# Kernel optimization log

Measured on AMD Instinct MI355X. Metric: run time of the kernel, lower is better.

The kernel has to match this reference:

```python
import jax, jax.numpy as jnp
import numpy as np

PAIR = 128
HID = 64
EPS = 1e-5


def _ln(x, w, b):
    mu = jnp.mean(x, axis=-1, keepdims=True)
    var = jnp.mean((x - mu) ** 2, axis=-1, keepdims=True)
    return (x - mu) * jax.lax.rsqrt(var + EPS) * w + b


def setup_inputs() -> dict:
    key = jax.random.key(0)
    ks = jax.random.split(key, 8)
    B, N = 1, 448
    s_in = 1.0 / np.sqrt(PAIR)
    s_h = 1.0 / np.sqrt(HID)
    return {
        "z": jax.random.normal(ks[0], (B, N, N, PAIR), jnp.float32),
        "z_mask": jnp.ones((B, N, N), jnp.float32),
        "ln_w": jnp.ones((PAIR,), jnp.float32),
        "ln_b": jnp.zeros((PAIR,), jnp.float32),
        "lnh_w": jnp.ones((HID,), jnp.float32),
        "lnh_b": jnp.zeros((HID,), jnp.float32),
        "g1_w": jax.random.uniform(ks[1], (PAIR, HID), jnp.float32, -s_in, s_in),
        "g1_b": jnp.zeros((HID,), jnp.float32),
        "g2_w": jax.random.uniform(ks[2], (PAIR, HID), jnp.float32, -s_in, s_in),
        "g2_b": jnp.zeros((HID,), jnp.float32),
        "l1_w": jax.random.uniform(ks[3], (PAIR, HID), jnp.float32, -s_in, s_in),
        "l1_b": jnp.zeros((HID,), jnp.float32),
        "l2_w": jax.random.uniform(ks[4], (PAIR, HID), jnp.float32, -s_in, s_in),
        "l2_b": jnp.zeros((HID,), jnp.float32),
        "eg_w": jax.random.uniform(ks[5], (PAIR, PAIR), jnp.float32, -s_in, s_in),
        "eg_b": jnp.zeros((PAIR,), jnp.float32),
        "out_w": jax.random.uniform(ks[6], (HID, PAIR), jnp.float32, -s_h, s_h),
        "out_b": jnp.zeros((PAIR,), jnp.float32),
    }


def reference(z, z_mask, ln_w, ln_b, lnh_w, lnh_b, g1_w, g1_b, g2_w, g2_b,
              l1_w, l1_b, l2_w, l2_b, eg_w, eg_b, out_w, out_b):
    m = z_mask[..., None]                      # [B,N,N,1]
    zn = _ln(z, ln_w, ln_b)                    # [B,N,N,P]
    ab1 = jax.nn.sigmoid(zn @ g1_w + g1_b) * (zn @ l1_w + l1_b) * m  # [B,N,N,H]
    ab2 = jax.nn.sigmoid(zn @ g2_w + g2_b) * (zn @ l2_w + l2_b) * m  # [B,N,N,H]
    # outgoing + incoming triangle products, per channel c
    block = (jnp.einsum('bikc,bjkc->bijc', ab1, ab2)
             + jnp.einsum('bkic,bkjc->bijc', ab1, ab2))              # [B,N,N,H]
    out = jax.nn.sigmoid(zn @ eg_w + eg_b) * (_ln(block, lnh_w, lnh_b) @ out_w + out_b) * m
    return out
```

## Files before the change

kernel.cpp:

```cpp
#include <hip/hip_runtime.h>
#include <stdint.h>

#define N 448
#define NN (N*N)
#define P 128
#define H 64
#define PN 512
#define CH (PN*N)

typedef __attribute__((ext_vector_type(8))) short bf16x8;
typedef __attribute__((ext_vector_type(4))) float f32x4;

__device__ __forceinline__ ushort f2bf(float f) {
    uint u = __builtin_bit_cast(uint, f);
    uint r = u + 0x7FFFu + ((u >> 16) & 1u);
    return (ushort)(r >> 16);
}
__device__ __forceinline__ float bf2f(ushort h) {
    uint u = ((uint)h) << 16;
    return __builtin_bit_cast(float, u);
}
__device__ __forceinline__ float sigmoidf(float x) {
    return 1.0f / (1.0f + __expf(-x));
}

__global__ void k_prep(const float* __restrict__ g1w, const float* __restrict__ l1w,
                       const float* __restrict__ g2w, const float* __restrict__ l2w,
                       const float* __restrict__ egw,
                       ushort* __restrict__ wfrag) {
    int idx = blockIdx.x*256 + threadIdx.x;
    for (int e = idx; e < 24*4*64*8; e += gridDim.x*256) {
        int b  = e & 7;
        int l  = (e >> 3) & 63;
        int ks = (e >> 9) & 3;
        int ct = e >> 11;
        int k   = ks*32 + 8*(l>>4) + b;
        int col = ct*16 + (l & 15);
        float v;
        if (col < 64)       v = g1w[k*64 + col];
        else if (col < 128) v = l1w[k*64 + col - 64];
        else if (col < 192) v = g2w[k*64 + col - 128];
        else if (col < 256) v = l2w[k*64 + col - 192];
        else                v = egw[k*128 + col - 256];
        wfrag[e] = f2bf(v);
    }
}

__global__ __launch_bounds__(256) void k_proj(
    const float* __restrict__ z, const float* __restrict__ mask,
    const float* __restrict__ lnw, const float* __restrict__ lnb,
    const float* __restrict__ g1b, const float* __restrict__ l1b,
    const float* __restrict__ g2b, const float* __restrict__ l2b,
    const float* __restrict__ egb,
    const ushort* __restrict__ wfrag,
    ushort* __restrict__ abt, ushort* __restrict__ gsig)
{
    __shared__ ushort zn[64*128];
    __shared__ ushort gs[64][136];
    const int t = threadIdx.x;
    const int w = t >> 6, l = t & 63;
    const int i = blockIdx.x / 7, j0 = (blockIdx.x % 7) * 64;

    {
        const int p = t >> 2;
        const int q = t & 3;
        const float* zp = z + (size_t)(i*N + j0 + p)*P + q*32;
        float4 v[8];
        #pragma unroll
        for (int x = 0; x < 8; ++x) v[x] = *(const float4*)(zp + x*4);
        float s = 0.f, sq = 0.f;
        #pragma unroll
        for (int x = 0; x < 8; ++x) {
            s  += v[x].x + v[x].y + v[x].z + v[x].w;
            sq += v[x].x*v[x].x + v[x].y*v[x].y + v[x].z*v[x].z + v[x].w*v[x].w;
        }
        s += __shfl_xor(s, 1);  sq += __shfl_xor(sq, 1);
        s += __shfl_xor(s, 2);  sq += __shfl_xor(sq, 2);
        float mu   = s * (1.0f/128.0f);
        float var  = sq * (1.0f/128.0f) - mu*mu;
        float rstd = rsqrtf(var + 1e-5f);
        #pragma unroll
        for (int cc = 0; cc < 4; ++cc) {
            int chunk = q*4 + cc;
            const float* lwp = lnw + chunk*8;
            const float* lbp = lnb + chunk*8;
            float4 lwa = *(const float4*)(lwp), lwb = *(const float4*)(lwp+4);
            float4 lba = *(const float4*)(lbp), lbb = *(const float4*)(lbp+4);
            float4 va = v[cc*2], vb = v[cc*2+1];
            float n0 = (va.x - mu)*rstd*lwa.x + lba.x;
            float n1 = (va.y - mu)*rstd*lwa.y + lba.y;
            float n2 = (va.z - mu)*rstd*lwa.z + lba.z;
            float n3 = (va.w - mu)*rstd*lwa.w + lba.w;
            float n4 = (vb.x - mu)*rstd*lwb.x + lbb.x;
            float n5 = (vb.y - mu)*rstd*lwb.y + lbb.y;
            float n6 = (vb.z - mu)*rstd*lwb.z + lbb.z;
            float n7 = (vb.w - mu)*rstd*lwb.w + lbb.w;
            uint4 pk;
            pk.x = (uint)f2bf(n0) | ((uint)f2bf(n1) << 16);
            pk.y = (uint)f2bf(n2) | ((uint)f2bf(n3) << 16);
            pk.z = (uint)f2bf(n4) | ((uint)f2bf(n5) << 16);
            pk.w = (uint)f2bf(n6) | ((uint)f2bf(n7) << 16);
            uint boff = (uint)p*256u + (((uint)(chunk ^ (p & 7)) & 15u) << 4);
            *(uint4*)((char*)zn + boff) = pk;
        }
    }
    __syncthreads();

    const int half = w & 1, pair = w >> 1;
    const uint lr = l & 15, lk = l >> 4;
    const float* mrow = mask + (size_t)i*N + j0;
    const float* gb = pair ? g2b : g1b;
    const float* lb = pair ? l2b : l1b;

    #pragma unroll 1
    for (int sub = 0; sub < 2; ++sub) {
        const int ctg = pair*8 + half*2 + sub;
        const int ctl = ctg + 4;
        f32x4 ag[4], al[4];
        #pragma unroll
        for (int mi = 0; mi < 4; ++mi) { ag[mi] = (f32x4){0,0,0,0}; al[mi] = (f32x4){0,0,0,0}; }

        #pragma unroll
        for (int ks = 0; ks < 4; ++ks) {
            bf16x8 bg = *(const bf16x8*)(wfrag + ((size_t)(ctg*4 + ks)*64 + l)*8);
            bf16x8 blf = *(const bf16x8*)(wfrag + ((size_t)(ctl*4 + ks)*64 + l)*8);
            #pragma unroll
            for (int mi = 0; mi < 4; ++mi) {
                uint row = mi*16u + lr;
                uint chunk = (uint)(ks*4) + lk;
                bf16x8 af = *(const bf16x8*)((const char*)zn + row*256u + (((chunk ^ (row & 7u)) & 15u) << 4));
                ag[mi] = __builtin_amdgcn_mfma_f32_16x16x32_bf16(af, bg,  ag[mi], 0,0,0);
                al[mi] = __builtin_amdgcn_mfma_f32_16x16x32_bf16(af, blf, al[mi], 0,0,0);
            }
        }

        const int cidx = (half*2 + sub)*16 + (int)lr;
        const float gbias = gb[cidx];
        const float lbias = lb[cidx];
        #pragma unroll
        for (int mi = 0; mi < 4; ++mi) {
            float mv[4];
            #pragma unroll
            for (int r = 0; r < 4; ++r) mv[r] = mrow[mi*16 + (int)lk*4 + r];
            ushort4 pk;
            float o0 = sigmoidf(ag[mi][0] + gbias) * (al[mi][0] + lbias) * mv[0];
            float o1 = sigmoidf(ag[mi][1] + gbias) * (al[mi][1] + lbias) * mv[1];
            float o2 = sigmoidf(ag[mi][2] + gbias) * (al[mi][2] + lbias) * mv[2];
            float o3 = sigmoidf(ag[mi][3] + gbias) * (al[mi][3] + lbias) * mv[3];
            pk.x = f2bf(o0); pk.y = f2bf(o1); pk.z = f2bf(o2); pk.w = f2bf(o3);
            size_t off = (size_t)(pair*64 + cidx)*CH + (size_t)i*N + j0 + mi*16 + (int)lk*4;
            *(ushort4*)(abt + off) = pk;
        }
    }

    {
        f32x4 ae[4][2];
        #pragma unroll
        for (int mi = 0; mi < 4; ++mi) { ae[mi][0] = (f32x4){0,0,0,0}; ae[mi][1] = (f32x4){0,0,0,0}; }

        #pragma unroll
        for (int ks = 0; ks < 4; ++ks) {
            bf16x8 b0 = *(const bf16x8*)(wfrag + ((size_t)((16 + w*2)*4 + ks)*64 + l)*8);
            bf16x8 b1 = *(const bf16x8*)(wfrag + ((size_t)((17 + w*2)*4 + ks)*64 + l)*8);
            #pragma unroll
            for (int mi = 0; mi < 4; ++mi) {
                uint row = mi*16u + lr;
                uint chunk = (uint)(ks*4) + lk;
                bf16x8 af = *(const bf16x8*)((const char*)zn + row*256u + (((chunk ^ (row & 7u)) & 15u) << 4));
                ae[mi][0] = __builtin_amdgcn_mfma_f32_16x16x32_bf16(af, b0, ae[mi][0], 0,0,0);
                ae[mi][1] = __builtin_amdgcn_mfma_f32_16x16x32_bf16(af, b1, ae[mi][1], 0,0,0);
            }
        }

        float biasB[2];
        biasB[0] = egb[w*32 + (int)lr];
        biasB[1] = egb[w*32 + 16 + (int)lr];
        #pragma unroll
        for (int mi = 0; mi < 4; ++mi) {
            float mv[4];
            #pragma unroll
            for (int r = 0; r < 4; ++r) mv[r] = mrow[mi*16 + (int)lk*4 + r];
            #pragma unroll
            for (int e = 0; e < 2; ++e) {
                int cg = w*32 + e*16 + (int)lr;
                #pragma unroll
                for (int r = 0; r < 4; ++r) {
                    float sg = sigmoidf(ae[mi][e][r] + biasB[e]) * mv[r];
                    gs[mi*16 + (int)lk*4 + r][cg] = f2bf(sg);
                }
            }
        }
    }
    __syncthreads();

    {
        int p2 = t >> 2, q2 = t & 3;
        size_t pos = (size_t)(i*N + j0 + p2);
        #pragma unroll
        for (int s2 = 0; s2 < 4; ++s2) {
            uint4 vv = *(const uint4*)((const char*)&gs[p2][0] + q2*64 + s2*16);
            *(uint4*)(gsig + pos*128 + q2*32 + s2*8) = vv;
        }
    }
}

__global__ __launch_bounds__(256) void k_transpose(const ushort* __restrict__ abt,
                                                   ushort* __restrict__ abtt) {
    int bid = blockIdx.x;
    int tile = bid % 49, a = bid / 49;
    int y0 = (tile / 7) * 64, x0 = (tile % 7) * 64;
    const ushort* src = abt  + (size_t)a*CH;
    ushort*       dst = abtt + (size_t)a*CH;
    __shared__ ushort tl[64][68];
    int t = threadIdx.x;
    #pragma unroll
    for (int q = 0; q < 4; ++q) {
        int f = q*1024 + t*4;
        int r = f >> 6, c4 = f & 63;
        ushort4 v = *(const ushort4*)(src + (size_t)(y0 + r)*N + x0 + c4);
        tl[r][c4] = v.x; tl[r][c4+1] = v.y; tl[r][c4+2] = v.z; tl[r][c4+3] = v.w;
    }
    __syncthreads();
    #pragma unroll
    for (int q = 0; q < 4; ++q) {
        int f = q*1024 + t*4;
        int r = f >> 6, c4 = f & 63;
        ushort4 v;
        v.x = tl[c4][r]; v.y = tl[c4+1][r]; v.z = tl[c4+2][r]; v.w = tl[c4+3][r];
        *(ushort4*)(dst + (size_t)(x0 + r)*N + y0 + c4) = v;
    }
}

__global__ __launch_bounds__(512) void k_tri(const ushort* __restrict__ abt,
                                             const ushort* __restrict__ abtt,
                                             float* __restrict__ blk) {
    int bid = (blockIdx.x & 7)*128 + (blockIdx.x >> 3);
    const int c = bid >> 4;
    const int tij = bid & 15;
    const int i0 = (tij >> 2) * 128, j0 = (tij & 3) * 128;
    const int t = threadIdx.x, w = t >> 6, l = t & 63;
    const int wr = w >> 2, wc = w & 3;
    const uint lr = l & 15, lk = l >> 4;

    __shared__ ushort lds[4][128*64];

    const int tt = w >> 1;
    const ushort* basep = (tt >= 2) ? abtt : abt;
    const int chan = (tt & 1) ? 64 + c : c;
    const int r0   = (tt & 1) ? j0 : i0;
    const ushort* sbase = basep + (size_t)chan*CH + (size_t)r0*N;
    const int rhalf = (w & 1) * 64;

    f32x4 acc[4][2];
    #pragma unroll
    for (int a = 0; a < 4; ++a) { acc[a][0] = (f32x4){0,0,0,0}; acc[a][1] = (f32x4){0,0,0,0}; }

    for (int kk = 0; kk < 7; ++kk) {
        __syncthreads();
        const ushort* sb = sbase + kk*64;
        #pragma unroll
        for (int q = 0; q < 8; ++q) {
            int r  = rhalf + q*8 + (l >> 3);
            int ch = (l & 7) ^ (r & 7);
            const ushort* g = sb + (size_t)r*N + ch*8;
            __builtin_amdgcn_global_load_lds(
                (const __attribute__((address_space(1))) uint*)g,
                (__attribute__((address_space(3))) uint*)(&lds[tt][rhalf*64 + q*512]),
                16, 0, 0);
        }
        __syncthreads();

        #pragma unroll
        for (int ks = 0; ks < 2; ++ks) {
            const uint chunk = (uint)(ks*4) + lk;
            bf16x8 a1[4], b1[2];
            #pragma unroll
            for (int x = 0; x < 4; ++x) {
                uint rowa = (uint)wr*64u + (uint)x*16u + lr;
                a1[x] = *(const bf16x8*)((const char*)lds[0] + rowa*128u + (((chunk ^ (rowa & 7u)) & 15u) << 4));
            }
            #pragma unroll
            for (int x = 0; x < 2; ++x) {
                uint rowb = (uint)wc*32u + (uint)x*16u + lr;
                b1[x] = *(const bf16x8*)((const char*)lds[1] + rowb*128u + (((chunk ^ (rowb & 7u)) & 15u) << 4));
            }
            #pragma unroll
            for (int mi = 0; mi < 4; ++mi)
                #pragma unroll
                for (int nj = 0; nj < 2; ++nj)
                    acc[mi][nj] = __builtin_amdgcn_mfma_f32_16x16x32_bf16(a1[mi], b1[nj], acc[mi][nj], 0,0,0);

            bf16x8 a2[4], b2[2];
            #pragma unroll
            for (int x = 0; x < 4; ++x) {
                uint rowa = (uint)wr*64u + (uint)x*16u + lr;
                a2[x] = *(const bf16x8*)((const char*)lds[2] + rowa*128u + (((chunk ^ (rowa & 7u)) & 15u) << 4));
            }
            #pragma unroll
            for (int x = 0; x < 2; ++x) {
                uint rowb = (uint)wc*32u + (uint)x*16u + lr;
                b2[x] = *(const bf16x8*)((const char*)lds[3] + rowb*128u + (((chunk ^ (rowb & 7u)) & 15u) << 4));
            }
            #pragma unroll
            for (int mi = 0; mi < 4; ++mi)
                #pragma unroll
                for (int nj = 0; nj < 2; ++nj)
                    acc[mi][nj] = __builtin_amdgcn_mfma_f32_16x16x32_bf16(a2[mi], b2[nj], acc[mi][nj], 0,0,0);
        }
    }

    #pragma unroll
    for (int mi = 0; mi < 4; ++mi) {
        int ib = i0 + wr*64 + mi*16 + (int)lk*4;
        #pragma unroll
        for (int nj = 0; nj < 2; ++nj) {
            int jb = j0 + wc*32 + nj*16 + (int)lr;
            if (jb < N) {
                #pragma unroll
                for (int r = 0; r < 4; ++r) {
                    int ii = ib + r;
                    if (ii < N) blk[(size_t)c*NN + (size_t)ii*N + jb] = acc[mi][nj][r];
                }
            }
        }
    }
}

__global__ __launch_bounds__(256) void k_out(const float* __restrict__ blk,
    const ushort* __restrict__ gsig,
    const float* __restrict__ lnhw, const float* __restrict__ lnhb,
    const float* __restrict__ outw, const float* __restrict__ outb,
    float* __restrict__ out)
{
    __shared__ float sblk[64][68];
    const int t = threadIdx.x;
    const int w = t >> 6, l = t & 63;
    const int pos0 = blockIdx.x * 64;

    #pragma unroll
    for (int q = 0; q < 4; ++q) {
        int flat = q*256 + t;
        int h = flat >> 4, f4 = flat & 15;
        float4 v = *(const float4*)(blk + (size_t)h*NN + pos0 + f4*4);
        sblk[f4*4+0][h] = v.x;
        sblk[f4*4+1][h] = v.y;
        sblk[f4*4+2][h] = v.z;
        sblk[f4*4+3][h] = v.w;
    }
    __syncthreads();

    {
        int p = w*16 + (l >> 2);
        int sub = l & 3;
        float vv[16];
        float s = 0.f, sq = 0.f;
        #pragma unroll
        for (int j = 0; j < 16; ++j) {
            float x = sblk[p][sub*16 + j];
            vv[j] = x; s += x; sq += x*x;
        }
        s += __shfl_xor(s, 1);  sq += __shfl_xor(sq, 1);
        s += __shfl_xor(s, 2);  sq += __shfl_xor(sq, 2);
        float mu   = s * (1.0f/64.0f);
        float var  = sq * (1.0f/64.0f) - mu*mu;
        float rstd = rsqrtf(var + 1e-5f);
        #pragma unroll
        for (int j = 0; j < 16; ++j) {
            float nv = (vv[j] - mu)*rstd*lnhw[sub*16+j] + lnhb[sub*16+j];
            sblk[p][sub*16 + j] = nv;
        }
    }
    __syncthreads();

    const int c4 = (t & 31) * 4;
    const int pg = t >> 5;
    float4 ob = *(const float4*)(outb + c4);

    #pragma unroll 1
    for (int hh = 0; hh < 2; ++hh) {
        const int prow = hh*32 + pg*4;
        float acc[4][4];
        #pragma unroll
        for (int j2 = 0; j2 < 4; ++j2)
            #pragma unroll
            for (int cc = 0; cc < 4; ++cc) acc[j2][cc] = 0.f;

        #pragma unroll 4
        for (int h4 = 0; h4 < 16; ++h4) {
            float4 wv[4];
            #pragma unroll
            for (int j = 0; j < 4; ++j)
                wv[j] = *(const float4*)(outw + (h4*4+j)*128 + c4);
            #pragma unroll
            for (int j2 = 0; j2 < 4; ++j2) {
                float4 av = *(const float4*)(&sblk[prow + j2][h4*4]);
                acc[j2][0] += av.x*wv[0].x + av.y*wv[1].x + av.z*wv[2].x + av.w*wv[3].x;
                acc[j2][1] += av.x*wv[0].y + av.y*wv[1].y + av.z*wv[2].y + av.w*wv[3].y;
                acc[j2][2] += av.x*wv[0].z + av.y*wv[1].z + av.z*wv[2].z + av.w*wv[3].z;
                acc[j2][3] += av.x*wv[0].w + av.y*wv[1].w + av.z*wv[2].w + av.w*wv[3].w;
            }
        }

        #pragma unroll
        for (int j2 = 0; j2 < 4; ++j2) {
            size_t pos = (size_t)(pos0 + prow + j2);
            ushort4 gv = *(const ushort4*)(gsig + pos*128 + c4);
            float4 res;
            res.x = bf2f(gv.x) * (acc[j2][0] + ob.x);
            res.y = bf2f(gv.y) * (acc[j2][1] + ob.y);
            res.z = bf2f(gv.z) * (acc[j2][2] + ob.z);
            res.w = bf2f(gv.w) * (acc[j2][3] + ob.w);
            *(float4*)(out + pos*128 + c4) = res;
        }
    }
}

extern "C" void kernel_launch(void* const* d_in, const int* in_sizes, int n_in,
                              void* d_out, int out_size, void* d_ws, size_t ws_size,
                              hipStream_t stream) {
    const float* z    = (const float*)d_in[0];
    const float* mask = (const float*)d_in[1];
    const float* lnw  = (const float*)d_in[2];
    const float* lnb  = (const float*)d_in[3];
    const float* lnhw = (const float*)d_in[4];
    const float* lnhb = (const float*)d_in[5];
    const float* g1w  = (const float*)d_in[6];
    const float* g1b  = (const float*)d_in[7];
    const float* g2w  = (const float*)d_in[8];
    const float* g2b  = (const float*)d_in[9];
    const float* l1w  = (const float*)d_in[10];
    const float* l1b  = (const float*)d_in[11];
    const float* l2w  = (const float*)d_in[12];
    const float* l2b  = (const float*)d_in[13];
    const float* egw  = (const float*)d_in[14];
    const float* egb  = (const float*)d_in[15];
    const float* outw = (const float*)d_in[16];
    const float* outb = (const float*)d_in[17];

    char* ws = (char*)d_ws;
    const size_t SZ_AB = (size_t)2*64*CH*2;
    const size_t SZ_G  = (size_t)NN*128*2;
    const size_t SZ_BL = (size_t)64*NN*4;
    ushort* abt    = (ushort*)ws;
    ushort* abtt   = (ushort*)(ws + SZ_AB);
    ushort* gsig   = (ushort*)(ws + 2*SZ_AB);
    float*  blkb   = (float*) (ws + 2*SZ_AB + SZ_G);
    ushort* wfrag  = (ushort*)(ws + 2*SZ_AB + SZ_G + SZ_BL);

    k_prep<<<32, 256, 0, stream>>>(g1w, l1w, g2w, l2w, egw, wfrag);
    k_proj<<<3136, 256, 0, stream>>>(z, mask, lnw, lnb, g1b, l1b, g2b, l2b, egb, wfrag, abt, gsig);
    k_transpose<<<128*49, 256, 0, stream>>>(abt, abtt);
    k_tri<<<64*16, 512, 0, stream>>>(abt, abtt, blkb);
    k_out<<<NN/64, 256, 0, stream>>>(blkb, gsig, lnhw, lnhb, outw, outb, (float*)d_out);
}
```

Baseline: 297.7 us.

## Enlarge per-wave tile in triangle kernel and streamline projection epilogues

The triangle-product kernel now runs 256 threads per block instead of 512. Each wave computes a 64x64 output tile (4x4 MFMA accumulators) rather than 64x32, which raises MFMA-to-LDS-read reuse and removes the cross-wave split of the staging loads. In the projection kernel, the manual bf16 rounding is replaced by the packed hardware convert instruction, mask loads become float4 vector loads, and the separate gating staging buffer is dropped by reusing the swizzled zn LDS region after an added barrier. The larger accumulator tile raises register pressure and halves threads per block, which may reduce occupancy or latency hiding.

Result: no change. 293.1 us (-1.6%).

```diff
diff --git a/kernel.cpp b/kernel.cpp
--- a/kernel.cpp
+++ b/kernel.cpp
@@ -22,6 +22,11 @@
 }
 __device__ __forceinline__ float sigmoidf(float x) {
     return 1.0f / (1.0f + __expf(-x));
+}
+__device__ __forceinline__ uint cvtpk(float lo, float hi) {
+    uint r;
+    asm("v_cvt_pk_bf16_f32 %0, %1, %2" : "=v"(r) : "v"(lo), "v"(hi));
+    return r;
 }
 
 __global__ void k_prep(const float* __restrict__ g1w, const float* __restrict__ l1w,
@@ -56,7 +61,6 @@
     ushort* __restrict__ abt, ushort* __restrict__ gsig)
 {
     __shared__ ushort zn[64*128];
-    __shared__ ushort gs[64][136];
     const int t = threadIdx.x;
     const int w = t >> 6, l = t & 63;
     const int i = blockIdx.x / 7, j0 = (blockIdx.x % 7) * 64;
@@ -96,10 +100,10 @@
             float n6 = (vb.z - mu)*rstd*lwb.z + lbb.z;
             float n7 = (vb.w - mu)*rstd*lwb.w + lbb.w;
             uint4 pk;
-            pk.x = (uint)f2bf(n0) | ((uint)f2bf(n1) << 16);
-            pk.y = (uint)f2bf(n2) | ((uint)f2bf(n3) << 16);
-            pk.z = (uint)f2bf(n4) | ((uint)f2bf(n5) << 16);
-            pk.w = (uint)f2bf(n6) | ((uint)f2bf(n7) << 16);
+            pk.x = cvtpk(n0, n1);
+            pk.y = cvtpk(n2, n3);
+            pk.z = cvtpk(n4, n5);
+            pk.w = cvtpk(n6, n7);
             uint boff = (uint)p*256u + (((uint)(chunk ^ (p & 7)) & 15u) << 4);
             *(uint4*)((char*)zn + boff) = pk;
         }
@@ -122,7 +126,7 @@
 
         #pragma unroll
         for (int ks = 0; ks < 4; ++ks) {
-            bf16x8 bg = *(const bf16x8*)(wfrag + ((size_t)(ctg*4 + ks)*64 + l)*8);
+            bf16x8 bg  = *(const bf16x8*)(wfrag + ((size_t)(ctg*4 + ks)*64 + l)*8);
             bf16x8 blf = *(const bf16x8*)(wfrag + ((size_t)(ctl*4 + ks)*64 + l)*8);
             #pragma unroll
             for (int mi = 0; mi < 4; ++mi) {
@@ -139,17 +143,16 @@
         const float lbias = lb[cidx];
         #pragma unroll
         for (int mi = 0; mi < 4; ++mi) {
-            float mv[4];
-            #pragma unroll
-            for (int r = 0; r < 4; ++r) mv[r] = mrow[mi*16 + (int)lk*4 + r];
-            ushort4 pk;
-            float o0 = sigmoidf(ag[mi][0] + gbias) * (al[mi][0] + lbias) * mv[0];
-            float o1 = sigmoidf(ag[mi][1] + gbias) * (al[mi][1] + lbias) * mv[1];
-            float o2 = sigmoidf(ag[mi][2] + gbias) * (al[mi][2] + lbias) * mv[2];
-            float o3 = sigmoidf(ag[mi][3] + gbias) * (al[mi][3] + lbias) * mv[3];
-            pk.x = f2bf(o0); pk.y = f2bf(o1); pk.z = f2bf(o2); pk.w = f2bf(o3);
+            float4 mv = *(const float4*)(mrow + mi*16 + (int)lk*4);
+            float o0 = sigmoidf(ag[mi][0] + gbias) * (al[mi][0] + lbias) * mv.x;
+            float o1 = sigmoidf(ag[mi][1] + gbias) * (al[mi][1] + lbias) * mv.y;
+            float o2 = sigmoidf(ag[mi][2] + gbias) * (al[mi][2] + lbias) * mv.z;
+            float o3 = sigmoidf(ag[mi][3] + gbias) * (al[mi][3] + lbias) * mv.w;
+            uint2 pk;
+            pk.x = cvtpk(o0, o1);
+            pk.y = cvtpk(o2, o3);
             size_t off = (size_t)(pair*64 + cidx)*CH + (size_t)i*N + j0 + mi*16 + (int)lk*4;
-            *(ushort4*)(abt + off) = pk;
+            *(uint2*)(abt + off) = pk;
         }
     }
 
@@ -172,21 +175,24 @@
             }
         }
 
+        __syncthreads();
+
         float biasB[2];
         biasB[0] = egb[w*32 + (int)lr];
         biasB[1] = egb[w*32 + 16 + (int)lr];
         #pragma unroll
         for (int mi = 0; mi < 4; ++mi) {
-            float mv[4];
-            #pragma unroll
-            for (int r = 0; r < 4; ++r) mv[r] = mrow[mi*16 + (int)lk*4 + r];
+            float4 mv = *(const float4*)(mrow + mi*16 + (int)lk*4);
+            float mva[4] = { mv.x, mv.y, mv.z, mv.w };
             #pragma unroll
             for (int e = 0; e < 2; ++e) {
-                int cg = w*32 + e*16 + (int)lr;
+                uint cg = (uint)(w*32 + e*16) + lr;
                 #pragma unroll
                 for (int r = 0; r < 4; ++r) {
-                    float sg = sigmoidf(ae[mi][e][r] + biasB[e]) * mv[r];
-                    gs[mi*16 + (int)lk*4 + r][cg] = f2bf(sg);
+                    float sg = sigmoidf(ae[mi][e][r] + biasB[e]) * mva[r];
+                    uint row = (uint)(mi*16) + lk*4u + (uint)r;
+                    uint boff = row*256u + (((((cg >> 3) ^ (row & 7u)) & 15u)) << 4) + ((cg & 7u) << 1);
+                    *(ushort*)((char*)zn + boff) = (ushort)cvtpk(sg, sg);
                 }
             }
         }
@@ -198,7 +204,9 @@
         size_t pos = (size_t)(i*N + j0 + p2);
         #pragma unroll
         for (int s2 = 0; s2 < 4; ++s2) {
-            uint4 vv = *(const uint4*)((const char*)&gs[p2][0] + q2*64 + s2*16);
+            int chunk = q2*4 + s2;
+            uint boff = (uint)p2*256u + (((uint)(chunk ^ (p2 & 7)) & 15u) << 4);
+            uint4 vv = *(const uint4*)((const char*)zn + boff);
             *(uint4*)(gsig + pos*128 + q2*32 + s2*8) = vv;
         }
     }
@@ -231,7 +239,7 @@
     }
 }
 
-__global__ __launch_bounds__(512) void k_tri(const ushort* __restrict__ abt,
+__global__ __launch_bounds__(256) void k_tri(const ushort* __restrict__ abt,
                                              const ushort* __restrict__ abtt,
                                              float* __restrict__ blk) {
     int bid = (blockIdx.x & 7)*128 + (blockIdx.x >> 3);
@@ -239,33 +247,33 @@
     const int tij = bid & 15;
     const int i0 = (tij >> 2) * 128, j0 = (tij & 3) * 128;
     const int t = threadIdx.x, w = t >> 6, l = t & 63;
-    const int wr = w >> 2, wc = w & 3;
+    const int wr = w >> 1, wc = w & 1;
     const uint lr = l & 15, lk = l >> 4;
 
     __shared__ ushort lds[4][128*64];
 
-    const int tt = w >> 1;
-    const ushort* basep = (tt >= 2) ? abtt : abt;
-    const int chan = (tt & 1) ? 64 + c : c;
-    const int r0   = (tt & 1) ? j0 : i0;
+    const ushort* basep = (w >= 2) ? abtt : abt;
+    const int chan = (w & 1) ? 64 + c : c;
+    const int r0   = (w & 1) ? j0 : i0;
     const ushort* sbase = basep + (size_t)chan*CH + (size_t)r0*N;
-    const int rhalf = (w & 1) * 64;
-
-    f32x4 acc[4][2];
+
+    f32x4 acc[4][4];
     #pragma unroll
-    for (int a = 0; a < 4; ++a) { acc[a][0] = (f32x4){0,0,0,0}; acc[a][1] = (f32x4){0,0,0,0}; }
+    for (int a = 0; a < 4; ++a)
+        #pragma unroll
+        for (int b = 0; b < 4; ++b) acc[a][b] = (f32x4){0.f,0.f,0.f,0.f};
 
     for (int kk = 0; kk < 7; ++kk) {
         __syncthreads();
         const ushort* sb = sbase + kk*64;
         #pragma unroll
-        for (int q = 0; q < 8; ++q) {
-            int r  = rhalf + q*8 + (l >> 3);
+        for (int q = 0; q < 16; ++q) {
+            int r  = q*8 + (l >> 3);
             int ch = (l & 7) ^ (r & 7);
             const ushort* g = sb + (size_t)r*N + ch*8;
             __builtin_amdgcn_global_load_lds(
                 (const __attribute__((address_space(1))) uint*)g,
-                (__attribute__((address_space(3))) uint*)(&lds[tt][rhalf*64 + q*512]),
+                (__attribute__((address_space(3))) uint*)(&lds[w][q*512]),
                 16, 0, 0);
         }
         __syncthreads();
@@ -273,38 +281,32 @@
         #pragma unroll
         for (int ks = 0; ks < 2; ++ks) {
             const uint chunk = (uint)(ks*4) + lk;
-            bf16x8 a1[4], b1[2];
+            bf16x8 a1[4], b1[4];
             #pragma unroll
             for (int x = 0; x < 4; ++x) {
                 uint rowa = (uint)wr*64u + (uint)x*16u + lr;
+                uint rowb = (uint)wc*64u + (uint)x*16u + lr;
                 a1[x] = *(const bf16x8*)((const char*)lds[0] + rowa*128u + (((chunk ^ (rowa & 7u)) & 15u) << 4));
-            }
-            #pragma unroll
-            for (int x = 0; x < 2; ++x) {
-                uint rowb = (uint)wc*32u + (uint)x*16u + lr;
                 b1[x] = *(const bf16x8*)((const char*)lds[1] + rowb*128u + (((chunk ^ (rowb & 7u)) & 15u) << 4));
             }
             #pragma unroll
             for (int mi = 0; mi < 4; ++mi)
                 #pragma unroll
-                for (int nj = 0; nj < 2; ++nj)
+                for (int nj = 0; nj < 4; ++nj)
                     acc[mi][nj] = __builtin_amdgcn_mfma_f32_16x16x32_bf16(a1[mi], b1[nj], acc[mi][nj], 0,0,0);
 
-            bf16x8 a2[4], b2[2];
+            bf16x8 a2[4], b2[4];
             #pragma unroll
             for (int x = 0; x < 4; ++x) {
                 uint rowa = (uint)wr*64u + (uint)x*16u + lr;
+                uint rowb = (uint)wc*64u + (uint)x*16u + lr;
                 a2[x] = *(const bf16x8*)((const char*)lds[2] + rowa*128u + (((chunk ^ (rowa & 7u)) & 15u) << 4));
-            }
-            #pragma unroll
-            for (int x = 0; x < 2; ++x) {
-                uint rowb = (uint)wc*32u + (uint)x*16u + lr;
                 b2[x] = *(const bf16x8*)((const char*)lds[3] + rowb*128u + (((chunk ^ (rowb & 7u)) & 15u) << 4));
             }
             #pragma unroll
             for (int mi = 0; mi < 4; ++mi)
                 #pragma unroll
-                for (int nj = 0; nj < 2; ++nj)
+                for (int nj = 0; nj < 4; ++nj)
                     acc[mi][nj] = __builtin_amdgcn_mfma_f32_16x16x32_bf16(a2[mi], b2[nj], acc[mi][nj], 0,0,0);
         }
     }
@@ -313,8 +315,8 @@
     for (int mi = 0; mi < 4; ++mi) {
         int ib = i0 + wr*64 + mi*16 + (int)lk*4;
         #pragma unroll
-        for (int nj = 0; nj < 2; ++nj) {
-            int jb = j0 + wc*32 + nj*16 + (int)lr;
+        for (int nj = 0; nj < 4; ++nj) {
+            int jb = j0 + wc*64 + nj*16 + (int)lr;
             if (jb < N) {
                 #pragma unroll
                 for (int r = 0; r < 4; ++r) {
@@ -450,6 +452,6 @@
     k_prep<<<32, 256, 0, stream>>>(g1w, l1w, g2w, l2w, egw, wfrag);
     k_proj<<<3136, 256, 0, stream>>>(z, mask, lnw, lnb, g1b, l1b, g2b, l2b, egb, wfrag, abt, gsig);
     k_transpose<<<128*49, 256, 0, stream>>>(abt, abtt);
-    k_tri<<<64*16, 512, 0, stream>>>(abt, abtt, blkb);
+    k_tri<<<64*16, 256, 0, stream>>>(abt, abtt, blkb);
     k_out<<<NN/64, 256, 0, stream>>>(blkb, gsig, lnhw, lnhb, outw, outb, (float*)d_out);
 }
```
